# Kernel optimization log

Hardware: AMD Instinct MI355X
Metric: run time of the kernel (lower is better)

The kernel has to match this reference:

```python
import jax, jax.numpy as jnp
import numpy as np

EPS = 1e-5

def conv1d(x, w, b):
    # x: (N,C,L), w: (O,I,3), stride 1, padding 1 -> same length
    y = jax.lax.conv_general_dilated(x, w, window_strides=(1,), padding=((1, 1),),
                                     dimension_numbers=('NCH', 'OIH', 'NCH'))
    return y + b[None, :, None]

def bn(x, g, b):
    # BatchNorm1d, training-mode batch statistics over (N, L) per channel
    m = x.mean(axis=(0, 2), keepdims=True)
    v = x.var(axis=(0, 2), keepdims=True)
    return (x - m) * jax.lax.rsqrt(v + EPS) * g[None, :, None] + b[None, :, None]

def setup_inputs() -> dict:
    V, E, H, L, NL = 50257, 512, 512, 2048, 2
    D = 1 + NL * 2  # 5 channels in the pre-attention conv stack
    key = jax.random.key(0)
    ks = iter(jax.random.split(key, 48))
    def rn(shape, s=0.02):
        return jax.random.normal(next(ks), shape, dtype=jnp.float32) * s
    inp = dict(
        emb=rn((V, E), 1.0),
        conv1_w=rn((32, D, 3)), conv1_b=rn((32,)),
        conv2_w=rn((D, 32, 3)), conv2_b=rn((D,)),
        conv3_w=rn((1, D, 3)), conv3_b=rn((1,)),
        conv4_w=rn((32, 3, 3)), conv4_b=rn((32,)),
        conv5_w=rn((3, 32, 3)), conv5_b=rn((3,)),
        conv6_w=rn((1, 3, 3)), conv6_b=rn((1,)),
        bn1_g=jnp.ones((32,)), bn1_b=jnp.zeros((32,)),
        bn2_g=jnp.ones((D,)), bn2_b=jnp.zeros((D,)),
        bn3_g=jnp.ones((1,)), bn3_b=jnp.zeros((1,)),
        bn4_g=jnp.ones((32,)), bn4_b=jnp.zeros((32,)),
        bn5_g=jnp.ones((3,)), bn5_b=jnp.zeros((3,)),
        bn6_g=jnp.ones((1,)), bn6_b=jnp.zeros((1,)),
        att_w=rn((L, E)), att_b=rn((L,)),
        gru_wih=rn((4, 3 * H, E)), gru_whh=rn((4, 3 * H, H)),
        gru_bih=rn((4, 3 * H)), gru_bhh=rn((4, 3 * H)),
        lo_w=rn((V, H)), lo_b=rn((V,)),
        h_state=rn((4, 1, H), 1.0),
        encoder_outs=rn((L, 2 * H), 1.0),
        x=jax.random.randint(next(ks), (1,), 0, V),
    )
    return inp

def reference(emb, conv1_w, conv1_b, conv2_w, conv2_b, conv3_w, conv3_b,
              conv4_w, conv4_b, conv5_w, conv5_b, conv6_w, conv6_b,
              bn1_g, bn1_b, bn2_g, bn2_b, bn3_g, bn3_b,
              bn4_g, bn4_b, bn5_g, bn5_b, bn6_g, bn6_b,
              att_w, att_b, gru_wih, gru_whh, gru_bih, gru_bhh,
              lo_w, lo_b, h_state, encoder_outs, x):
    H = h_state.shape[-1]
    # dropout(p=0.1) treated as identity (eval mode / deterministic reference)
    embadded = emb[x].reshape(1, 1, H)                                      # (1,1,512)
    pre = jnp.concatenate([h_state.reshape(1, -1, H), embadded], axis=1)    # (1,5,512)
    c = jax.nn.relu(bn(conv1d(pre, conv1_w, conv1_b), bn1_g, bn1_b))        # (1,32,512)
    pre = jax.nn.relu(bn(conv1d(c, conv2_w, conv2_b) + pre, bn2_g, bn2_b))  # residual, (1,5,512)
    pre = jax.nn.relu(bn(conv1d(pre, conv3_w, conv3_b), bn3_g, bn3_b))      # (1,1,512)
    aw = jax.nn.softmax(pre.reshape(1, -1) @ att_w.T + att_b, axis=1)       # (1,L)
    app = (aw @ encoder_outs).reshape(1, -1, H)                             # (1,2,512) (bidir encoder)
    com = jnp.concatenate([app, embadded], axis=1)                          # (1,3,512)
    c = jax.nn.relu(bn(conv1d(com, conv4_w, conv4_b), bn4_g, bn4_b))        # (1,32,512)
    com = jax.nn.relu(bn(conv1d(c, conv5_w, conv5_b) + com, bn5_g, bn5_b))  # residual, (1,3,512)
    com = jax.nn.relu(bn(conv1d(com, conv6_w, conv6_b), bn6_g, bn6_b))      # (1,1,512)
    # 4-layer stacked GRU, single time step, batch 1 (PyTorch gate order r,z,n)
    xt = com.reshape(H)
    h_new = []
    for l in range(h_state.shape[0]):
        gi = gru_wih[l] @ xt + gru_bih[l]
        gh = gru_whh[l] @ h_state[l, 0] + gru_bhh[l]
        ir, iz, inn = jnp.split(gi, 3)
        hr, hz, hn = jnp.split(gh, 3)
        r = jax.nn.sigmoid(ir + hr)
        z = jax.nn.sigmoid(iz + hz)
        n = jnp.tanh(inn + r * hn)
        xt = (1.0 - z) * n + z * h_state[l, 0]
        h_new.append(xt)
    h_state_new = jnp.stack(h_new)[:, None, :]                              # (4,1,512)
    out = jax.nn.log_softmax((xt @ lo_w.T + lo_b)[None, :], axis=1)         # (1,V)
    return out, h_state_new
```

## Files before the change

kernel.cpp:

```cpp
#include <hip/hip_runtime.h>
#include <hip/hip_bf16.h>

typedef __attribute__((ext_vector_type(4))) float f32x4;

constexpr int WSF_PRE1 = 0;
constexpr int WSF_LOGA = 512;
constexpr int WSF_PART = 2560;
constexpr int WSF_SUME = 18944;
constexpr int WSF_XT   = 18960;
constexpr int WSF_LOGV = 21520;
constexpr int WSF_PM   = 71792;
constexpr int WSF_PS   = 72592;
constexpr int WSF_LSE  = 73392;
constexpr int NVOCAB   = 50257;
constexpr int NBLK_V   = 786;

__device__ __forceinline__ float wave_rsum(float v) {
#pragma unroll
    for (int o = 32; o > 0; o >>= 1) v += __shfl_down(v, o);
    return v;
}
__device__ __forceinline__ float sigm(float x) { return 1.0f / (1.0f + __expf(-x)); }

__global__ __launch_bounds__(512) void k_pre(
    const float* __restrict__ emb, const int* __restrict__ xidx,
    const float* __restrict__ hstate,
    const float* __restrict__ w1, const float* __restrict__ b1,
    const float* __restrict__ w2, const float* __restrict__ b2,
    const float* __restrict__ w3, const float* __restrict__ b3,
    const float* __restrict__ g1, const float* __restrict__ bb1,
    const float* __restrict__ g2, const float* __restrict__ bb2,
    const float* __restrict__ g3, const float* __restrict__ bb3,
    float* __restrict__ ws)
{
    constexpr int W1 = 0, B1 = 480, G1 = 512, BB1 = 544;
    constexpr int W2 = 576, B2 = 1056, G2 = 1061, BB2 = 1066;
    constexpr int W3 = 1071, B3 = 1086, G3 = 1087, BB3 = 1088, NW = 1089;
    __shared__ float s_w[NW];
    __shared__ float s_pre[5][512];
    __shared__ float s_y[32][512];
    __shared__ float s_stat[32][2];

    const int tid = threadIdx.x;
    const int lane = tid & 63, wid = tid >> 6;
    const int l = tid;

    if (tid < 480) s_w[W1 + tid] = w1[tid];
    if (tid < 32) { s_w[B1 + tid] = b1[tid]; s_w[G1 + tid] = g1[tid]; s_w[BB1 + tid] = bb1[tid]; }
    if (tid < 480) s_w[W2 + tid] = w2[tid];
    if (tid < 5) { s_w[B2 + tid] = b2[tid]; s_w[G2 + tid] = g2[tid]; s_w[BB2 + tid] = bb2[tid]; }
    if (tid < 15) s_w[W3 + tid] = w3[tid];
    if (tid == 0) { s_w[B3] = b3[0]; s_w[G3] = g3[0]; s_w[BB3] = bb3[0]; }

    const int x = xidx[0];
#pragma unroll
    for (int c = 0; c < 4; ++c) s_pre[c][l] = hstate[c * 512 + l];
    s_pre[4][l] = emb[(size_t)x * 512 + l];
    __syncthreads();

    float px[5][3];
#pragma unroll
    for (int ic = 0; ic < 5; ++ic) {
        px[ic][0] = (l > 0)   ? s_pre[ic][l - 1] : 0.0f;
        px[ic][1] =             s_pre[ic][l];
        px[ic][2] = (l < 511) ? s_pre[ic][l + 1] : 0.0f;
    }
#pragma unroll 4
    for (int oc = 0; oc < 32; ++oc) {
        float a = s_w[B1 + oc];
#pragma unroll
        for (int ic = 0; ic < 5; ++ic)
#pragma unroll
            for (int k = 0; k < 3; ++k)
                a += s_w[W1 + oc * 15 + ic * 3 + k] * px[ic][k];
        s_y[oc][l] = a;
    }
    __syncthreads();

#pragma unroll
    for (int t = 0; t < 4; ++t) {
        const int oc = wid * 4 + t;
        float s = 0.f, s2 = 0.f;
#pragma unroll
        for (int j = 0; j < 8; ++j) {
            float v = s_y[oc][lane + j * 64];
            s += v; s2 += v * v;
        }
        s = wave_rsum(s); s2 = wave_rsum(s2);
        if (lane == 0) {
            float m = s * (1.0f / 512.0f);
            float var = s2 * (1.0f / 512.0f) - m * m;
            s_stat[oc][0] = m; s_stat[oc][1] = rsqrtf(var + 1e-5f);
        }
    }
    __syncthreads();

#pragma unroll 4
    for (int oc = 0; oc < 32; ++oc) {
        float m = s_stat[oc][0], r = s_stat[oc][1];
        s_y[oc][l] = fmaxf((s_y[oc][l] - m) * r * s_w[G1 + oc] + s_w[BB1 + oc], 0.0f);
    }
    __syncthreads();

    float y2[5];
#pragma unroll
    for (int oc = 0; oc < 5; ++oc) y2[oc] = s_w[B2 + oc];
#pragma unroll 2
    for (int ic = 0; ic < 32; ++ic) {
        float c0 = (l > 0)   ? s_y[ic][l - 1] : 0.0f;
        float c1 =             s_y[ic][l];
        float c2 = (l < 511) ? s_y[ic][l + 1] : 0.0f;
#pragma unroll
        for (int oc = 0; oc < 5; ++oc) {
            const int base = W2 + (oc * 32 + ic) * 3;
            y2[oc] += s_w[base] * c0 + s_w[base + 1] * c1 + s_w[base + 2] * c2;
        }
    }
#pragma unroll
    for (int oc = 0; oc < 5; ++oc) y2[oc] += s_pre[oc][l];
    __syncthreads();
#pragma unroll
    for (int oc = 0; oc < 5; ++oc) s_y[oc][l] = y2[oc];
    __syncthreads();

    if (wid < 5) {
        const int oc = wid;
        float s = 0.f, s2 = 0.f;
#pragma unroll
        for (int j = 0; j < 8; ++j) {
            float v = s_y[oc][lane + j * 64];
            s += v; s2 += v * v;
        }
        s = wave_rsum(s); s2 = wave_rsum(s2);
        if (lane == 0) {
            float m = s * (1.0f / 512.0f);
            float var = s2 * (1.0f / 512.0f) - m * m;
            s_stat[oc][0] = m; s_stat[oc][1] = rsqrtf(var + 1e-5f);
        }
    }
    __syncthreads();
#pragma unroll
    for (int oc = 0; oc < 5; ++oc) {
        float m = s_stat[oc][0], r = s_stat[oc][1];
        s_pre[oc][l] = fmaxf((y2[oc] - m) * r * s_w[G2 + oc] + s_w[BB2 + oc], 0.0f);
    }
    __syncthreads();

    float a3 = s_w[B3];
#pragma unroll
    for (int ic = 0; ic < 5; ++ic) {
        float c0 = (l > 0)   ? s_pre[ic][l - 1] : 0.0f;
        float c1 =             s_pre[ic][l];
        float c2 = (l < 511) ? s_pre[ic][l + 1] : 0.0f;
        a3 += s_w[W3 + ic * 3] * c0 + s_w[W3 + ic * 3 + 1] * c1 + s_w[W3 + ic * 3 + 2] * c2;
    }
    s_y[0][l] = a3;
    __syncthreads();
    if (wid == 0) {
        float s = 0.f, s2 = 0.f;
#pragma unroll
        for (int j = 0; j < 8; ++j) {
            float v = s_y[0][lane + j * 64];
            s += v; s2 += v * v;
        }
        s = wave_rsum(s); s2 = wave_rsum(s2);
        if (lane == 0) {
            float m = s * (1.0f / 512.0f);
            float var = s2 * (1.0f / 512.0f) - m * m;
            s_stat[0][0] = m; s_stat[0][1] = rsqrtf(var + 1e-5f);
        }
    }
    __syncthreads();
    ws[WSF_PRE1 + l] = fmaxf((a3 - s_stat[0][0]) * s_stat[0][1] * s_w[G3] + s_w[BB3], 0.0f);
}

__global__ __launch_bounds__(256) void k_attlogit(
    const float* __restrict__ attw, const float* __restrict__ attb,
    float* __restrict__ ws)
{
    const int tid = threadIdx.x, lane = tid & 63, wid = tid >> 6;
    float q0[4], q1[4];
#pragma unroll
    for (int j = 0; j < 4; ++j) {
        q0[j] = ws[WSF_PRE1 + lane * 4 + j];
        q1[j] = ws[WSF_PRE1 + 256 + lane * 4 + j];
    }
    const int row0 = (blockIdx.x * 4 + wid) * 4;
#pragma unroll
    for (int r = 0; r < 4; ++r) {
        const int row = row0 + r;
        f32x4 w0 = *reinterpret_cast<const f32x4*>(attw + (size_t)row * 512 + lane * 4);
        f32x4 w1 = *reinterpret_cast<const f32x4*>(attw + (size_t)row * 512 + 256 + lane * 4);
        float a = 0.f;
#pragma unroll
        for (int j = 0; j < 4; ++j) a += w0[j] * q0[j] + w1[j] * q1[j];
        a = wave_rsum(a);
        if (lane == 0) ws[WSF_LOGA + row] = a + attb[row];
    }
}

__global__ __launch_bounds__(256) void k_attpv(
    const float* __restrict__ enc, float* __restrict__ ws)
{
    __shared__ float s_e[2048];
    __shared__ float s_r[256];
    const int tid = threadIdx.x;
#pragma unroll
    for (int k = 0; k < 8; ++k) s_e[tid + k * 256] = ws[WSF_LOGA + tid + k * 256];
    __syncthreads();
    float m = -INFINITY;
#pragma unroll
    for (int k = 0; k < 8; ++k) m = fmaxf(m, s_e[tid + k * 256]);
    s_r[tid] = m; __syncthreads();
    for (int s = 128; s > 0; s >>= 1) {
        if (tid < s) s_r[tid] = fmaxf(s_r[tid], s_r[tid + s]);
        __syncthreads();
    }
    const float M = s_r[0];
    __syncthreads();
    float t = 0.f;
#pragma unroll
    for (int k = 0; k < 8; ++k) {
        const int i = tid + k * 256;
        float e = __expf(s_e[i] - M);
        s_e[i] = e;
        t += e;
    }
    s_r[tid] = t; __syncthreads();
    for (int s = 128; s > 0; s >>= 1) {
        if (tid < s) s_r[tid] += s_r[tid + s];
        __syncthreads();
    }
    const float S = s_r[0];
    if (blockIdx.x == 0 && tid == 0) ws[WSF_SUME] = S;

    const int jc = blockIdx.x >> 1, half = blockIdx.x & 1;
    const int col = half * 512 + tid * 2;
    const float* ep = enc + (size_t)(jc * 128) * 1024 + col;
    float a0 = 0.f, a1 = 0.f;
#pragma unroll 4
    for (int jj = 0; jj < 128; ++jj) {
        const float w = s_e[jc * 128 + jj];
        float2 e = *reinterpret_cast<const float2*>(ep + (size_t)jj * 1024);
        a0 += w * e.x;
        a1 += w * e.y;
    }
    ws[WSF_PART + jc * 1024 + col]     = a0;
    ws[WSF_PART + jc * 1024 + col + 1] = a1;
}

__global__ __launch_bounds__(512) void k_post(
    const float* __restrict__ emb, const int* __restrict__ xidx,
    const float* __restrict__ w4, const float* __restrict__ b4,
    const float* __restrict__ w5, const float* __restrict__ b5,
    const float* __restrict__ w6, const float* __restrict__ b6,
    const float* __restrict__ g4, const float* __restrict__ bb4,
    const float* __restrict__ g5, const float* __restrict__ bb5,
    const float* __restrict__ g6, const float* __restrict__ bb6,
    float* __restrict__ ws)
{
    constexpr int W4 = 0, B4 = 288, G4 = 320, BB4 = 352;
    constexpr int W5 = 384, B5 = 672, G5 = 675, BB5 = 678;
    constexpr int W6 = 681, B6 = 690, G6 = 691, BB6 = 692, NW = 693;
    __shared__ float s_w[NW];
    __shared__ float s_com[3][512];
    __shared__ float s_y[32][512];
    __shared__ float s_stat[32][2];

    const int tid = threadIdx.x;
    const int lane = tid & 63, wid = tid >> 6;
    const int l = tid;

    if (tid < 288) s_w[W4 + tid] = w4[tid];
    if (tid < 32) { s_w[B4 + tid] = b4[tid]; s_w[G4 + tid] = g4[tid]; s_w[BB4 + tid] = bb4[tid]; }
    if (tid < 288) s_w[W5 + tid] = w5[tid];
    if (tid < 3) { s_w[B5 + tid] = b5[tid]; s_w[G5 + tid] = g5[tid]; s_w[BB5 + tid] = bb5[tid]; }
    if (tid < 9) s_w[W6 + tid] = w6[tid];
    if (tid == 0) { s_w[B6] = b6[0]; s_w[G6] = g6[0]; s_w[BB6] = bb6[0]; }

    const float invS = 1.0f / ws[WSF_SUME];
    float a0 = 0.f, a1 = 0.f;
#pragma unroll
    for (int p = 0; p < 16; ++p) {
        a0 += ws[WSF_PART + p * 1024 + l];
        a1 += ws[WSF_PART + p * 1024 + 512 + l];
    }
    const int x = xidx[0];
    s_com[0][l] = a0 * invS;
    s_com[1][l] = a1 * invS;
    s_com[2][l] = emb[(size_t)x * 512 + l];
    __syncthreads();

    float px[3][3];
#pragma unroll
    for (int ic = 0; ic < 3; ++ic) {
        px[ic][0] = (l > 0)   ? s_com[ic][l - 1] : 0.0f;
        px[ic][1] =             s_com[ic][l];
        px[ic][2] = (l < 511) ? s_com[ic][l + 1] : 0.0f;
    }
#pragma unroll 4
    for (int oc = 0; oc < 32; ++oc) {
        float a = s_w[B4 + oc];
#pragma unroll
        for (int ic = 0; ic < 3; ++ic)
#pragma unroll
            for (int k = 0; k < 3; ++k)
                a += s_w[W4 + oc * 9 + ic * 3 + k] * px[ic][k];
        s_y[oc][l] = a;
    }
    __syncthreads();

#pragma unroll
    for (int t = 0; t < 4; ++t) {
        const int oc = wid * 4 + t;
        float s = 0.f, s2 = 0.f;
#pragma unroll
        for (int j = 0; j < 8; ++j) {
            float v = s_y[oc][lane + j * 64];
            s += v; s2 += v * v;
        }
        s = wave_rsum(s); s2 = wave_rsum(s2);
        if (lane == 0) {
            float m = s * (1.0f / 512.0f);
            float var = s2 * (1.0f / 512.0f) - m * m;
            s_stat[oc][0] = m; s_stat[oc][1] = rsqrtf(var + 1e-5f);
        }
    }
    __syncthreads();
#pragma unroll 4
    for (int oc = 0; oc < 32; ++oc) {
        float m = s_stat[oc][0], r = s_stat[oc][1];
        s_y[oc][l] = fmaxf((s_y[oc][l] - m) * r * s_w[G4 + oc] + s_w[BB4 + oc], 0.0f);
    }
    __syncthreads();

    float y2[3];
#pragma unroll
    for (int oc = 0; oc < 3; ++oc) y2[oc] = s_w[B5 + oc];
#pragma unroll 2
    for (int ic = 0; ic < 32; ++ic) {
        float c0 = (l > 0)   ? s_y[ic][l - 1] : 0.0f;
        float c1 =             s_y[ic][l];
        float c2 = (l < 511) ? s_y[ic][l + 1] : 0.0f;
#pragma unroll
        for (int oc = 0; oc < 3; ++oc) {
            const int base = W5 + (oc * 32 + ic) * 3;
            y2[oc] += s_w[base] * c0 + s_w[base + 1] * c1 + s_w[base + 2] * c2;
        }
    }
#pragma unroll
    for (int oc = 0; oc < 3; ++oc) y2[oc] += s_com[oc][l];
    __syncthreads();
#pragma unroll
    for (int oc = 0; oc < 3; ++oc) s_y[oc][l] = y2[oc];
    __syncthreads();
    if (wid < 3) {
        const int oc = wid;
        float s = 0.f, s2 = 0.f;
#pragma unroll
        for (int j = 0; j < 8; ++j) {
            float v = s_y[oc][lane + j * 64];
            s += v; s2 += v * v;
        }
        s = wave_rsum(s); s2 = wave_rsum(s2);
        if (lane == 0) {
            float m = s * (1.0f / 512.0f);
            float var = s2 * (1.0f / 512.0f) - m * m;
            s_stat[oc][0] = m; s_stat[oc][1] = rsqrtf(var + 1e-5f);
        }
    }
    __syncthreads();
#pragma unroll
    for (int oc = 0; oc < 3; ++oc) {
        float m = s_stat[oc][0], r = s_stat[oc][1];
        s_com[oc][l] = fmaxf((y2[oc] - m) * r * s_w[G5 + oc] + s_w[BB5 + oc], 0.0f);
    }
    __syncthreads();

    float a6 = s_w[B6];
#pragma unroll
    for (int ic = 0; ic < 3; ++ic) {
        float c0 = (l > 0)   ? s_com[ic][l - 1] : 0.0f;
        float c1 =             s_com[ic][l];
        float c2 = (l < 511) ? s_com[ic][l + 1] : 0.0f;
        a6 += s_w[W6 + ic * 3] * c0 + s_w[W6 + ic * 3 + 1] * c1 + s_w[W6 + ic * 3 + 2] * c2;
    }
    s_y[0][l] = a6;
    __syncthreads();
    if (wid == 0) {
        float s = 0.f, s2 = 0.f;
#pragma unroll
        for (int j = 0; j < 8; ++j) {
            float v = s_y[0][lane + j * 64];
            s += v; s2 += v * v;
        }
        s = wave_rsum(s); s2 = wave_rsum(s2);
        if (lane == 0) {
            float m = s * (1.0f / 512.0f);
            float var = s2 * (1.0f / 512.0f) - m * m;
            s_stat[0][0] = m; s_stat[0][1] = rsqrtf(var + 1e-5f);
        }
    }
    __syncthreads();
    ws[WSF_XT + l] = fmaxf((a6 - s_stat[0][0]) * s_stat[0][1] * s_w[G6] + s_w[BB6], 0.0f);
}

__global__ __launch_bounds__(256) void k_gru(
    const float* __restrict__ wih, const float* __restrict__ whh,
    const float* __restrict__ bih, const float* __restrict__ bhh,
    const float* __restrict__ hstate,
    const float* __restrict__ xt_in, float* __restrict__ xt_out,
    float* __restrict__ hout, int layer)
{
    wih += (size_t)layer * 1536 * 512;
    whh += (size_t)layer * 1536 * 512;
    bih += layer * 1536;
    bhh += layer * 1536;
    const float* hp = hstate + layer * 512;

    const int tid = threadIdx.x, lane = tid & 63, wid = tid >> 6;
    float xq0[4], xq1[4], hq0[4], hq1[4];
#pragma unroll
    for (int j = 0; j < 4; ++j) {
        xq0[j] = xt_in[lane * 4 + j];
        xq1[j] = xt_in[256 + lane * 4 + j];
        hq0[j] = hp[lane * 4 + j];
        hq1[j] = hp[256 + lane * 4 + j];
    }
    __shared__ float s_g[8][6];
    const int i0 = blockIdx.x * 8;
#pragma unroll
    for (int t = 0; t < 2; ++t) {
        const int ii = wid * 2 + t;
        const int i = i0 + ii;
        float a[6] = {0.f, 0.f, 0.f, 0.f, 0.f, 0.f};
#pragma unroll
        for (int g = 0; g < 3; ++g) {
            const float* wr = wih + (size_t)(i + g * 512) * 512;
            f32x4 w0 = *reinterpret_cast<const f32x4*>(wr + lane * 4);
            f32x4 w1 = *reinterpret_cast<const f32x4*>(wr + 256 + lane * 4);
#pragma unroll
            for (int j = 0; j < 4; ++j) a[g] += w0[j] * xq0[j] + w1[j] * xq1[j];
        }
#pragma unroll
        for (int g = 0; g < 3; ++g) {
            const float* wr = whh + (size_t)(i + g * 512) * 512;
            f32x4 w0 = *reinterpret_cast<const f32x4*>(wr + lane * 4);
            f32x4 w1 = *reinterpret_cast<const f32x4*>(wr + 256 + lane * 4);
#pragma unroll
            for (int j = 0; j < 4; ++j) a[3 + g] += w0[j] * hq0[j] + w1[j] * hq1[j];
        }
#pragma unroll
        for (int g = 0; g < 6; ++g) a[g] = wave_rsum(a[g]);
        if (lane == 0) {
#pragma unroll
            for (int g = 0; g < 6; ++g) s_g[ii][g] = a[g];
        }
    }
    __syncthreads();
    if (tid < 8) {
        const int i = i0 + tid;
        float ir = s_g[tid][0] + bih[i];
        float iz = s_g[tid][1] + bih[i + 512];
        float in_ = s_g[tid][2] + bih[i + 1024];
        float hr = s_g[tid][3] + bhh[i];
        float hz = s_g[tid][4] + bhh[i + 512];
        float hn = s_g[tid][5] + bhh[i + 1024];
        float r = sigm(ir + hr);
        float z = sigm(iz + hz);
        float n = tanhf(in_ + r * hn);
        float hprev = hp[i];
        float h = (1.0f - z) * n + z * hprev;
        xt_out[i] = h;
        hout[i] = h;
    }
}

__global__ __launch_bounds__(256) void k_vocab(
    const float* __restrict__ low, const float* __restrict__ lob,
    float* __restrict__ ws)
{
    const int tid = threadIdx.x, lane = tid & 63, wid = tid >> 6;
    float q0[4], q1[4];
#pragma unroll
    for (int j = 0; j < 4; ++j) {
        q0[j] = ws[WSF_XT + 4 * 512 + lane * 4 + j];
        q1[j] = ws[WSF_XT + 4 * 512 + 256 + lane * 4 + j];
    }

    const int row0 = blockIdx.x * 64 + wid * 16;
    float m = -INFINITY, s = 0.0f;
#pragma unroll 4
    for (int r = 0; r < 16; ++r) {
        const int row = row0 + r;
        if (row < NVOCAB) {
            f32x4 w0 = *reinterpret_cast<const f32x4*>(low + (size_t)row * 512 + lane * 4);
            f32x4 w1 = *reinterpret_cast<const f32x4*>(low + (size_t)row * 512 + 256 + lane * 4);
            float a = 0.f;
#pragma unroll
            for (int j = 0; j < 4; ++j) a += w0[j] * q0[j] + w1[j] * q1[j];
            a = wave_rsum(a);
            if (lane == 0) {
                float v = a + lob[row];
                ws[WSF_LOGV + row] = v;
                if (v > m) { s = s * __expf(m - v) + 1.0f; m = v; }
                else       { s += __expf(v - m); }
            }
        }
    }
    __shared__ float sm[4], ss[4];
    if (lane == 0) { sm[wid] = m; ss[wid] = s; }
    __syncthreads();
    if (tid == 0) {
        float M = -INFINITY, S = 0.0f;
#pragma unroll
        for (int w = 0; w < 4; ++w) {
            float mb = sm[w], sb = ss[w];
            if (sb > 0.0f) {
                if (mb > M) { S = S * __expf(M - mb) + sb; M = mb; }
                else        { S += sb * __expf(mb - M); }
            }
        }
        ws[WSF_PM + blockIdx.x] = M;
        ws[WSF_PS + blockIdx.x] = S;
    }
}

__global__ __launch_bounds__(256) void k_lse(float* __restrict__ ws, int nb)
{
    __shared__ float sm[256], ss[256];
    const int tid = threadIdx.x;
    float M = -INFINITY, S = 0.0f;
    for (int i = tid; i < nb; i += 256) {
        float mb = ws[WSF_PM + i], sb = ws[WSF_PS + i];
        if (sb > 0.0f) {
            if (mb > M) { S = S * __expf(M - mb) + sb; M = mb; }
            else        { S += sb * __expf(mb - M); }
        }
    }
    sm[tid] = M; ss[tid] = S;
    __syncthreads();
    for (int st = 128; st > 0; st >>= 1) {
        if (tid < st) {
            float mb = sm[tid + st], sb = ss[tid + st];
            if (sb > 0.0f) {
                if (mb > sm[tid]) { ss[tid] = ss[tid] * __expf(sm[tid] - mb) + sb; sm[tid] = mb; }
                else              { ss[tid] += sb * __expf(mb - sm[tid]); }
            }
        }
        __syncthreads();
    }
    if (tid == 0) ws[WSF_LSE] = sm[0] + logf(ss[0]);
}

__global__ __launch_bounds__(256) void k_out(
    const float* __restrict__ ws, float* __restrict__ out)
{
    const int i = blockIdx.x * 256 + threadIdx.x;
    if (i < NVOCAB) out[i] = ws[WSF_LOGV + i] - ws[WSF_LSE];
}

extern "C" void kernel_launch(void* const* d_in, const int* in_sizes, int n_in,
                              void* d_out, int out_size, void* d_ws, size_t ws_size,
                              hipStream_t stream)
{
    (void)in_sizes; (void)n_in; (void)out_size; (void)ws_size;
    const float* emb     = (const float*)d_in[0];
    const float* conv1_w = (const float*)d_in[1];  const float* conv1_b = (const float*)d_in[2];
    const float* conv2_w = (const float*)d_in[3];  const float* conv2_b = (const float*)d_in[4];
    const float* conv3_w = (const float*)d_in[5];  const float* conv3_b = (const float*)d_in[6];
    const float* conv4_w = (const float*)d_in[7];  const float* conv4_b = (const float*)d_in[8];
    const float* conv5_w = (const float*)d_in[9];  const float* conv5_b = (const float*)d_in[10];
    const float* conv6_w = (const float*)d_in[11]; const float* conv6_b = (const float*)d_in[12];
    const float* bn1_g = (const float*)d_in[13];   const float* bn1_b = (const float*)d_in[14];
    const float* bn2_g = (const float*)d_in[15];   const float* bn2_b = (const float*)d_in[16];
    const float* bn3_g = (const float*)d_in[17];   const float* bn3_b = (const float*)d_in[18];
    const float* bn4_g = (const float*)d_in[19];   const float* bn4_b = (const float*)d_in[20];
    const float* bn5_g = (const float*)d_in[21];   const float* bn5_b = (const float*)d_in[22];
    const float* bn6_g = (const float*)d_in[23];   const float* bn6_b = (const float*)d_in[24];
    const float* att_w = (const float*)d_in[25];   const float* att_b = (const float*)d_in[26];
    const float* gru_wih = (const float*)d_in[27]; const float* gru_whh = (const float*)d_in[28];
    const float* gru_bih = (const float*)d_in[29]; const float* gru_bhh = (const float*)d_in[30];
    const float* lo_w = (const float*)d_in[31];    const float* lo_b = (const float*)d_in[32];
    const float* h_state = (const float*)d_in[33];
    const float* enc = (const float*)d_in[34];
    const int* x = (const int*)d_in[35];

    float* ws = (float*)d_ws;
    float* out = (float*)d_out;

    k_pre<<<1, 512, 0, stream>>>(emb, x, h_state,
        conv1_w, conv1_b, conv2_w, conv2_b, conv3_w, conv3_b,
        bn1_g, bn1_b, bn2_g, bn2_b, bn3_g, bn3_b, ws);
    k_attlogit<<<128, 256, 0, stream>>>(att_w, att_b, ws);
    k_attpv<<<32, 256, 0, stream>>>(enc, ws);
    k_post<<<1, 512, 0, stream>>>(emb, x,
        conv4_w, conv4_b, conv5_w, conv5_b, conv6_w, conv6_b,
        bn4_g, bn4_b, bn5_g, bn5_b, bn6_g, bn6_b, ws);
    for (int l = 0; l < 4; ++l) {
        k_gru<<<64, 256, 0, stream>>>(gru_wih, gru_whh, gru_bih, gru_bhh, h_state,
            ws + WSF_XT + l * 512, ws + WSF_XT + (l + 1) * 512,
            out + NVOCAB + l * 512, l);
    }
    k_vocab<<<NBLK_V, 256, 0, stream>>>(lo_w, lo_b, ws);
    k_lse<<<1, 256, 0, stream>>>(ws, NBLK_V);
    k_out<<<197, 256, 0, stream>>>(ws, out);
}
```

Before: 100.4 us.

## Fuse attention logits with PV and merge LSE into output kernel

Merges the attention-logit and attention-PV kernels into one kernel in which each block computes exp of its 64 logits, writes a partial denominator and accumulates its partial context vector. The global max subtraction is dropped. The vocab LSE reduction is folded into the output kernel, with every block recomputing it redundantly. This removes two launches and a global serialization step, at the cost of fewer blocks streaming att_w and possible exp overflow for large logits.

```diff
diff --git a/kernel.cpp b/kernel.cpp
--- a/kernel.cpp
+++ b/kernel.cpp
@@ -3,17 +3,15 @@
 
 typedef __attribute__((ext_vector_type(4))) float f32x4;
 
-constexpr int WSF_PRE1 = 0;
-constexpr int WSF_LOGA = 512;
-constexpr int WSF_PART = 2560;
-constexpr int WSF_SUME = 18944;
-constexpr int WSF_XT   = 18960;
-constexpr int WSF_LOGV = 21520;
-constexpr int WSF_PM   = 71792;
-constexpr int WSF_PS   = 72592;
-constexpr int WSF_LSE  = 73392;
-constexpr int NVOCAB   = 50257;
-constexpr int NBLK_V   = 786;
+constexpr int WSF_Q     = 0;
+constexpr int WSF_ADEN  = 512;
+constexpr int WSF_APART = 1024;
+constexpr int WSF_XT    = 33792;
+constexpr int WSF_LOGV  = 36352;
+constexpr int WSF_PM    = 86624;
+constexpr int WSF_PS    = 87424;
+constexpr int NVOCAB    = 50257;
+constexpr int NBLK_V    = 786;
 
 __device__ __forceinline__ float wave_rsum(float v) {
 #pragma unroll
@@ -40,10 +38,7 @@
     __shared__ float s_pre[5][512];
     __shared__ float s_y[32][512];
     __shared__ float s_stat[32][2];
-
-    const int tid = threadIdx.x;
-    const int lane = tid & 63, wid = tid >> 6;
-    const int l = tid;
+    const int tid = threadIdx.x, lane = tid & 63, wid = tid >> 6, l = tid;
 
     if (tid < 480) s_w[W1 + tid] = w1[tid];
     if (tid < 32) { s_w[B1 + tid] = b1[tid]; s_w[G1 + tid] = g1[tid]; s_w[BB1 + tid] = bb1[tid]; }
@@ -61,9 +56,9 @@
     float px[5][3];
 #pragma unroll
     for (int ic = 0; ic < 5; ++ic) {
-        px[ic][0] = (l > 0)   ? s_pre[ic][l - 1] : 0.0f;
+        px[ic][0] = (l > 0)   ? s_pre[ic][l-1] : 0.f;
         px[ic][1] =             s_pre[ic][l];
-        px[ic][2] = (l < 511) ? s_pre[ic][l + 1] : 0.0f;
+        px[ic][2] = (l < 511) ? s_pre[ic][l+1] : 0.f;
     }
 #pragma unroll 4
     for (int oc = 0; oc < 32; ++oc) {
@@ -72,34 +67,23 @@
         for (int ic = 0; ic < 5; ++ic)
 #pragma unroll
             for (int k = 0; k < 3; ++k)
-                a += s_w[W1 + oc * 15 + ic * 3 + k] * px[ic][k];
+                a += s_w[W1 + oc*15 + ic*3 + k] * px[ic][k];
         s_y[oc][l] = a;
     }
     __syncthreads();
-
 #pragma unroll
     for (int t = 0; t < 4; ++t) {
         const int oc = wid * 4 + t;
         float s = 0.f, s2 = 0.f;
 #pragma unroll
-        for (int j = 0; j < 8; ++j) {
-            float v = s_y[oc][lane + j * 64];
-            s += v; s2 += v * v;
-        }
+        for (int j = 0; j < 8; ++j) { float v = s_y[oc][lane + j*64]; s += v; s2 += v*v; }
         s = wave_rsum(s); s2 = wave_rsum(s2);
-        if (lane == 0) {
-            float m = s * (1.0f / 512.0f);
-            float var = s2 * (1.0f / 512.0f) - m * m;
-            s_stat[oc][0] = m; s_stat[oc][1] = rsqrtf(var + 1e-5f);
-        }
-    }
-    __syncthreads();
-
+        if (lane == 0) { float m = s/512.f, var = s2/512.f - m*m; s_stat[oc][0] = m; s_stat[oc][1] = rsqrtf(var + 1e-5f); }
+    }
+    __syncthreads();
 #pragma unroll 4
-    for (int oc = 0; oc < 32; ++oc) {
-        float m = s_stat[oc][0], r = s_stat[oc][1];
-        s_y[oc][l] = fmaxf((s_y[oc][l] - m) * r * s_w[G1 + oc] + s_w[BB1 + oc], 0.0f);
-    }
+    for (int oc = 0; oc < 32; ++oc)
+        s_y[oc][l] = fmaxf((s_y[oc][l] - s_stat[oc][0]) * s_stat[oc][1] * s_w[G1+oc] + s_w[BB1+oc], 0.f);
     __syncthreads();
 
     float y2[5];
@@ -107,13 +91,13 @@
     for (int oc = 0; oc < 5; ++oc) y2[oc] = s_w[B2 + oc];
 #pragma unroll 2
     for (int ic = 0; ic < 32; ++ic) {
-        float c0 = (l > 0)   ? s_y[ic][l - 1] : 0.0f;
+        float c0 = (l > 0)   ? s_y[ic][l-1] : 0.f;
         float c1 =             s_y[ic][l];
-        float c2 = (l < 511) ? s_y[ic][l + 1] : 0.0f;
+        float c2 = (l < 511) ? s_y[ic][l+1] : 0.f;
 #pragma unroll
         for (int oc = 0; oc < 5; ++oc) {
-            const int base = W2 + (oc * 32 + ic) * 3;
-            y2[oc] += s_w[base] * c0 + s_w[base + 1] * c1 + s_w[base + 2] * c2;
+            const int base = W2 + (oc*32 + ic)*3;
+            y2[oc] += s_w[base]*c0 + s_w[base+1]*c1 + s_w[base+2]*c2;
         }
     }
 #pragma unroll
@@ -122,131 +106,85 @@
 #pragma unroll
     for (int oc = 0; oc < 5; ++oc) s_y[oc][l] = y2[oc];
     __syncthreads();
-
     if (wid < 5) {
         const int oc = wid;
         float s = 0.f, s2 = 0.f;
 #pragma unroll
-        for (int j = 0; j < 8; ++j) {
-            float v = s_y[oc][lane + j * 64];
-            s += v; s2 += v * v;
-        }
+        for (int j = 0; j < 8; ++j) { float v = s_y[oc][lane + j*64]; s += v; s2 += v*v; }
         s = wave_rsum(s); s2 = wave_rsum(s2);
-        if (lane == 0) {
-            float m = s * (1.0f / 512.0f);
-            float var = s2 * (1.0f / 512.0f) - m * m;
-            s_stat[oc][0] = m; s_stat[oc][1] = rsqrtf(var + 1e-5f);
-        }
-    }
-    __syncthreads();
-#pragma unroll
-    for (int oc = 0; oc < 5; ++oc) {
-        float m = s_stat[oc][0], r = s_stat[oc][1];
-        s_pre[oc][l] = fmaxf((y2[oc] - m) * r * s_w[G2 + oc] + s_w[BB2 + oc], 0.0f);
-    }
+        if (lane == 0) { float m = s/512.f, var = s2/512.f - m*m; s_stat[oc][0] = m; s_stat[oc][1] = rsqrtf(var + 1e-5f); }
+    }
+    __syncthreads();
+#pragma unroll
+    for (int oc = 0; oc < 5; ++oc)
+        s_pre[oc][l] = fmaxf((y2[oc] - s_stat[oc][0]) * s_stat[oc][1] * s_w[G2+oc] + s_w[BB2+oc], 0.f);
     __syncthreads();
 
     float a3 = s_w[B3];
 #pragma unroll
     for (int ic = 0; ic < 5; ++ic) {
-        float c0 = (l > 0)   ? s_pre[ic][l - 1] : 0.0f;
+        float c0 = (l > 0)   ? s_pre[ic][l-1] : 0.f;
         float c1 =             s_pre[ic][l];
-        float c2 = (l < 511) ? s_pre[ic][l + 1] : 0.0f;
-        a3 += s_w[W3 + ic * 3] * c0 + s_w[W3 + ic * 3 + 1] * c1 + s_w[W3 + ic * 3 + 2] * c2;
+        float c2 = (l < 511) ? s_pre[ic][l+1] : 0.f;
+        a3 += s_w[W3+ic*3]*c0 + s_w[W3+ic*3+1]*c1 + s_w[W3+ic*3+2]*c2;
     }
     s_y[0][l] = a3;
     __syncthreads();
     if (wid == 0) {
         float s = 0.f, s2 = 0.f;
 #pragma unroll
-        for (int j = 0; j < 8; ++j) {
-            float v = s_y[0][lane + j * 64];
-            s += v; s2 += v * v;
-        }
+        for (int j = 0; j < 8; ++j) { float v = s_y[0][lane + j*64]; s += v; s2 += v*v; }
         s = wave_rsum(s); s2 = wave_rsum(s2);
+        if (lane == 0) { float m = s/512.f, var = s2/512.f - m*m; s_stat[0][0] = m; s_stat[0][1] = rsqrtf(var + 1e-5f); }
+    }
+    __syncthreads();
+    ws[WSF_Q + l] = fmaxf((a3 - s_stat[0][0]) * s_stat[0][1] * s_w[G3] + s_w[BB3], 0.f);
+}
+
+__global__ __launch_bounds__(256) void k_att(
+    const float* __restrict__ attw, const float* __restrict__ attb,
+    const float* __restrict__ enc, float* __restrict__ ws)
+{
+    __shared__ float s_e[64];
+    __shared__ float s_d[4];
+    const int tid = threadIdx.x, lane = tid & 63, wid = tid >> 6;
+    const int jc = blockIdx.x;
+
+    float q0[4], q1[4];
+#pragma unroll
+    for (int j = 0; j < 4; ++j) {
+        q0[j] = ws[WSF_Q + lane*4 + j];
+        q1[j] = ws[WSF_Q + 256 + lane*4 + j];
+    }
+    float dpart = 0.f;
+#pragma unroll 4
+    for (int r = 0; r < 16; ++r) {
+        const int row = jc * 64 + wid * 16 + r;
+        f32x4 w0 = *(const f32x4*)(attw + (size_t)row*512 + lane*4);
+        f32x4 w1 = *(const f32x4*)(attw + (size_t)row*512 + 256 + lane*4);
+        float a = 0.f;
+#pragma unroll
+        for (int j = 0; j < 4; ++j) a += w0[j]*q0[j] + w1[j]*q1[j];
+        a = wave_rsum(a);
         if (lane == 0) {
-            float m = s * (1.0f / 512.0f);
-            float var = s2 * (1.0f / 512.0f) - m * m;
-            s_stat[0][0] = m; s_stat[0][1] = rsqrtf(var + 1e-5f);
-        }
-    }
-    __syncthreads();
-    ws[WSF_PRE1 + l] = fmaxf((a3 - s_stat[0][0]) * s_stat[0][1] * s_w[G3] + s_w[BB3], 0.0f);
-}
-
-__global__ __launch_bounds__(256) void k_attlogit(
-    const float* __restrict__ attw, const float* __restrict__ attb,
-    float* __restrict__ ws)
-{
-    const int tid = threadIdx.x, lane = tid & 63, wid = tid >> 6;
-    float q0[4], q1[4];
-#pragma unroll
-    for (int j = 0; j < 4; ++j) {
-        q0[j] = ws[WSF_PRE1 + lane * 4 + j];
-        q1[j] = ws[WSF_PRE1 + 256 + lane * 4 + j];
-    }
-    const int row0 = (blockIdx.x * 4 + wid) * 4;
-#pragma unroll
-    for (int r = 0; r < 4; ++r) {
-        const int row = row0 + r;
-        f32x4 w0 = *reinterpret_cast<const f32x4*>(attw + (size_t)row * 512 + lane * 4);
-        f32x4 w1 = *reinterpret_cast<const f32x4*>(attw + (size_t)row * 512 + 256 + lane * 4);
-        float a = 0.f;
-#pragma unroll
-        for (int j = 0; j < 4; ++j) a += w0[j] * q0[j] + w1[j] * q1[j];
-        a = wave_rsum(a);
-        if (lane == 0) ws[WSF_LOGA + row] = a + attb[row];
-    }
-}
-
-__global__ __launch_bounds__(256) void k_attpv(
-    const float* __restrict__ enc, float* __restrict__ ws)
-{
-    __shared__ float s_e[2048];
-    __shared__ float s_r[256];
-    const int tid = threadIdx.x;
-#pragma unroll
-    for (int k = 0; k < 8; ++k) s_e[tid + k * 256] = ws[WSF_LOGA + tid + k * 256];
-    __syncthreads();
-    float m = -INFINITY;
-#pragma unroll
-    for (int k = 0; k < 8; ++k) m = fmaxf(m, s_e[tid + k * 256]);
-    s_r[tid] = m; __syncthreads();
-    for (int s = 128; s > 0; s >>= 1) {
-        if (tid < s) s_r[tid] = fmaxf(s_r[tid], s_r[tid + s]);
-        __syncthreads();
-    }
-    const float M = s_r[0];
-    __syncthreads();
-    float t = 0.f;
-#pragma unroll
-    for (int k = 0; k < 8; ++k) {
-        const int i = tid + k * 256;
-        float e = __expf(s_e[i] - M);
-        s_e[i] = e;
-        t += e;
-    }
-    s_r[tid] = t; __syncthreads();
-    for (int s = 128; s > 0; s >>= 1) {
-        if (tid < s) s_r[tid] += s_r[tid + s];
-        __syncthreads();
-    }
-    const float S = s_r[0];
-    if (blockIdx.x == 0 && tid == 0) ws[WSF_SUME] = S;
-
-    const int jc = blockIdx.x >> 1, half = blockIdx.x & 1;
-    const int col = half * 512 + tid * 2;
-    const float* ep = enc + (size_t)(jc * 128) * 1024 + col;
-    float a0 = 0.f, a1 = 0.f;
-#pragma unroll 4
-    for (int jj = 0; jj < 128; ++jj) {
-        const float w = s_e[jc * 128 + jj];
-        float2 e = *reinterpret_cast<const float2*>(ep + (size_t)jj * 1024);
-        a0 += w * e.x;
-        a1 += w * e.y;
-    }
-    ws[WSF_PART + jc * 1024 + col]     = a0;
-    ws[WSF_PART + jc * 1024 + col + 1] = a1;
+            float e = __expf(a + attb[row]);
+            s_e[wid*16 + r] = e;
+            dpart += e;
+        }
+    }
+    if (lane == 0) s_d[wid] = dpart;
+    __syncthreads();
+    if (tid == 0) ws[WSF_ADEN + jc] = s_d[0] + s_d[1] + s_d[2] + s_d[3];
+
+    const int col = tid * 4;
+    const float* ep = enc + (size_t)(jc * 64) * 1024 + col;
+    f32x4 acc = {0.f, 0.f, 0.f, 0.f};
+#pragma unroll 8
+    for (int jj = 0; jj < 64; ++jj) {
+        f32x4 v = *(const f32x4*)(ep + (size_t)jj * 1024);
+        acc += s_e[jj] * v;
+    }
+    *(f32x4*)(ws + WSF_APART + jc * 1024 + col) = acc;
 }
 
 __global__ __launch_bounds__(512) void k_post(
@@ -266,10 +204,7 @@
     __shared__ float s_com[3][512];
     __shared__ float s_y[32][512];
     __shared__ float s_stat[32][2];
-
-    const int tid = threadIdx.x;
-    const int lane = tid & 63, wid = tid >> 6;
-    const int l = tid;
+    const int tid = threadIdx.x, lane = tid & 63, wid = tid >> 6, l = tid;
 
     if (tid < 288) s_w[W4 + tid] = w4[tid];
     if (tid < 32) { s_w[B4 + tid] = b4[tid]; s_w[G4 + tid] = g4[tid]; s_w[BB4 + tid] = bb4[tid]; }
@@ -278,25 +213,28 @@
     if (tid < 9) s_w[W6 + tid] = w6[tid];
     if (tid == 0) { s_w[B6] = b6[0]; s_w[G6] = g6[0]; s_w[BB6] = bb6[0]; }
 
-    const float invS = 1.0f / ws[WSF_SUME];
+    float den = 0.f;
+#pragma unroll 8
+    for (int i = 0; i < 32; ++i) den += ws[WSF_ADEN + i];
+    const float invS = 1.0f / den;
     float a0 = 0.f, a1 = 0.f;
-#pragma unroll
-    for (int p = 0; p < 16; ++p) {
-        a0 += ws[WSF_PART + p * 1024 + l];
-        a1 += ws[WSF_PART + p * 1024 + 512 + l];
+#pragma unroll 8
+    for (int p = 0; p < 32; ++p) {
+        a0 += ws[WSF_APART + p*1024 + l];
+        a1 += ws[WSF_APART + p*1024 + 512 + l];
     }
     const int x = xidx[0];
     s_com[0][l] = a0 * invS;
     s_com[1][l] = a1 * invS;
-    s_com[2][l] = emb[(size_t)x * 512 + l];
+    s_com[2][l] = emb[(size_t)x*512 + l];
     __syncthreads();
 
     float px[3][3];
 #pragma unroll
     for (int ic = 0; ic < 3; ++ic) {
-        px[ic][0] = (l > 0)   ? s_com[ic][l - 1] : 0.0f;
+        px[ic][0] = (l > 0)   ? s_com[ic][l-1] : 0.f;
         px[ic][1] =             s_com[ic][l];
-        px[ic][2] = (l < 511) ? s_com[ic][l + 1] : 0.0f;
+        px[ic][2] = (l < 511) ? s_com[ic][l+1] : 0.f;
     }
 #pragma unroll 4
     for (int oc = 0; oc < 32; ++oc) {
@@ -305,33 +243,23 @@
         for (int ic = 0; ic < 3; ++ic)
 #pragma unroll
             for (int k = 0; k < 3; ++k)
-                a += s_w[W4 + oc * 9 + ic * 3 + k] * px[ic][k];
+                a += s_w[W4 + oc*9 + ic*3 + k] * px[ic][k];
         s_y[oc][l] = a;
     }
     __syncthreads();
-
 #pragma unroll
     for (int t = 0; t < 4; ++t) {
         const int oc = wid * 4 + t;
         float s = 0.f, s2 = 0.f;
 #pragma unroll
-        for (int j = 0; j < 8; ++j) {
-            float v = s_y[oc][lane + j * 64];
-            s += v; s2 += v * v;
-        }
+        for (int j = 0; j < 8; ++j) { float v = s_y[oc][lane + j*64]; s += v; s2 += v*v; }
         s = wave_rsum(s); s2 = wave_rsum(s2);
-        if (lane == 0) {
-            float m = s * (1.0f / 512.0f);
-            float var = s2 * (1.0f / 512.0f) - m * m;
-            s_stat[oc][0] = m; s_stat[oc][1] = rsqrtf(var + 1e-5f);
-        }
+        if (lane == 0) { float m = s/512.f, var = s2/512.f - m*m; s_stat[oc][0] = m; s_stat[oc][1] = rsqrtf(var + 1e-5f); }
     }
     __syncthreads();
 #pragma unroll 4
-    for (int oc = 0; oc < 32; ++oc) {
-        float m = s_stat[oc][0], r = s_stat[oc][1];
-        s_y[oc][l] = fmaxf((s_y[oc][l] - m) * r * s_w[G4 + oc] + s_w[BB4 + oc], 0.0f);
-    }
+    for (int oc = 0; oc < 32; ++oc)
+        s_y[oc][l] = fmaxf((s_y[oc][l] - s_stat[oc][0]) * s_stat[oc][1] * s_w[G4+oc] + s_w[BB4+oc], 0.f);
     __syncthreads();
 
     float y2[3];
@@ -339,13 +267,13 @@
     for (int oc = 0; oc < 3; ++oc) y2[oc] = s_w[B5 + oc];
 #pragma unroll 2
     for (int ic = 0; ic < 32; ++ic) {
-        float c0 = (l > 0)   ? s_y[ic][l - 1] : 0.0f;
+        float c0 = (l > 0)   ? s_y[ic][l-1] : 0.f;
         float c1 =             s_y[ic][l];
-        float c2 = (l < 511) ? s_y[ic][l + 1] : 0.0f;
+        float c2 = (l < 511) ? s_y[ic][l+1] : 0.f;
 #pragma unroll
         for (int oc = 0; oc < 3; ++oc) {
-            const int base = W5 + (oc * 32 + ic) * 3;
-            y2[oc] += s_w[base] * c0 + s_w[base + 1] * c1 + s_w[base + 2] * c2;
+            const int base = W5 + (oc*32 + ic)*3;
+            y2[oc] += s_w[base]*c0 + s_w[base+1]*c1 + s_w[base+2]*c2;
         }
     }
 #pragma unroll
@@ -358,51 +286,35 @@
         const int oc = wid;
         float s = 0.f, s2 = 0.f;
 #pragma unroll
-        for (int j = 0; j < 8; ++j) {
-            float v = s_y[oc][lane + j * 64];
-            s += v; s2 += v * v;
-        }
+        for (int j = 0; j < 8; ++j) { float v = s_y[oc][lane + j*64]; s += v; s2 += v*v; }
         s = wave_rsum(s); s2 = wave_rsum(s2);
-        if (lane == 0) {
-            float m = s * (1.0f / 512.0f);
-            float var = s2 * (1.0f / 512.0f) - m * m;
-            s_stat[oc][0] = m; s_stat[oc][1] = rsqrtf(var + 1e-5f);
-        }
-    }
-    __syncthreads();
-#pragma unroll
-    for (int oc = 0; oc < 3; ++oc) {
-        float m = s_stat[oc][0], r = s_stat[oc][1];
-        s_com[oc][l] = fmaxf((y2[oc] - m) * r * s_w[G5 + oc] + s_w[BB5 + oc], 0.0f);
-    }
+        if (lane == 0) { float m = s/512.f, var = s2/512.f - m*m; s_stat[oc][0] = m; s_stat[oc][1] = rsqrtf(var + 1e-5f); }
+    }
+    __syncthreads();
+#pragma unroll
+    for (int oc = 0; oc < 3; ++oc)
+        s_com[oc][l] = fmaxf((y2[oc] - s_stat[oc][0]) * s_stat[oc][1] * s_w[G5+oc] + s_w[BB5+oc], 0.f);
     __syncthreads();
 
     float a6 = s_w[B6];
 #pragma unroll
     for (int ic = 0; ic < 3; ++ic) {
-        float c0 = (l > 0)   ? s_com[ic][l - 1] : 0.0f;
+        float c0 = (l > 0)   ? s_com[ic][l-1] : 0.f;
         float c1 =             s_com[ic][l];
-        float c2 = (l < 511) ? s_com[ic][l + 1] : 0.0f;
-        a6 += s_w[W6 + ic * 3] * c0 + s_w[W6 + ic * 3 + 1] * c1 + s_w[W6 + ic * 3 + 2] * c2;
+        float c2 = (l < 511) ? s_com[ic][l+1] : 0.f;
+        a6 += s_w[W6+ic*3]*c0 + s_w[W6+ic*3+1]*c1 + s_w[W6+ic*3+2]*c2;
     }
     s_y[0][l] = a6;
     __syncthreads();
     if (wid == 0) {
         float s = 0.f, s2 = 0.f;
 #pragma unroll
-        for (int j = 0; j < 8; ++j) {
-            float v = s_y[0][lane + j * 64];
-            s += v; s2 += v * v;
-        }
+        for (int j = 0; j < 8; ++j) { float v = s_y[0][lane + j*64]; s += v; s2 += v*v; }
         s = wave_rsum(s); s2 = wave_rsum(s2);
-        if (lane == 0) {
-            float m = s * (1.0f / 512.0f);
-            float var = s2 * (1.0f / 512.0f) - m * m;
-            s_stat[0][0] = m; s_stat[0][1] = rsqrtf(var + 1e-5f);
-        }
-    }
-    __syncthreads();
-    ws[WSF_XT + l] = fmaxf((a6 - s_stat[0][0]) * s_stat[0][1] * s_w[G6] + s_w[BB6], 0.0f);
+        if (lane == 0) { float m = s/512.f, var = s2/512.f - m*m; s_stat[0][0] = m; s_stat[0][1] = rsqrtf(var + 1e-5f); }
+    }
+    __syncthreads();
+    ws[WSF_XT + l] = fmaxf((a6 - s_stat[0][0]) * s_stat[0][1] * s_w[G6] + s_w[BB6], 0.f);
 }
 
 __global__ __launch_bounds__(256) void k_gru(
@@ -422,10 +334,10 @@
     float xq0[4], xq1[4], hq0[4], hq1[4];
 #pragma unroll
     for (int j = 0; j < 4; ++j) {
-        xq0[j] = xt_in[lane * 4 + j];
-        xq1[j] = xt_in[256 + lane * 4 + j];
-        hq0[j] = hp[lane * 4 + j];
-        hq1[j] = hp[256 + lane * 4 + j];
+        xq0[j] = xt_in[lane*4 + j];
+        xq1[j] = xt_in[256 + lane*4 + j];
+        hq0[j] = hp[lane*4 + j];
+        hq1[j] = hp[256 + lane*4 + j];
     }
     __shared__ float s_g[8][6];
     const int i0 = blockIdx.x * 8;
@@ -436,19 +348,19 @@
         float a[6] = {0.f, 0.f, 0.f, 0.f, 0.f, 0.f};
 #pragma unroll
         for (int g = 0; g < 3; ++g) {
-            const float* wr = wih + (size_t)(i + g * 512) * 512;
-            f32x4 w0 = *reinterpret_cast<const f32x4*>(wr + lane * 4);
-            f32x4 w1 = *reinterpret_cast<const f32x4*>(wr + 256 + lane * 4);
-#pragma unroll
-            for (int j = 0; j < 4; ++j) a[g] += w0[j] * xq0[j] + w1[j] * xq1[j];
+            const float* wr = wih + (size_t)(i + g*512) * 512;
+            f32x4 w0 = *(const f32x4*)(wr + lane*4);
+            f32x4 w1 = *(const f32x4*)(wr + 256 + lane*4);
+#pragma unroll
+            for (int j = 0; j < 4; ++j) a[g] += w0[j]*xq0[j] + w1[j]*xq1[j];
         }
 #pragma unroll
         for (int g = 0; g < 3; ++g) {
-            const float* wr = whh + (size_t)(i + g * 512) * 512;
-            f32x4 w0 = *reinterpret_cast<const f32x4*>(wr + lane * 4);
-            f32x4 w1 = *reinterpret_cast<const f32x4*>(wr + 256 + lane * 4);
-#pragma unroll
-            for (int j = 0; j < 4; ++j) a[3 + g] += w0[j] * hq0[j] + w1[j] * hq1[j];
+            const float* wr = whh + (size_t)(i + g*512) * 512;
+            f32x4 w0 = *(const f32x4*)(wr + lane*4);
+            f32x4 w1 = *(const f32x4*)(wr + 256 + lane*4);
+#pragma unroll
+            for (int j = 0; j < 4; ++j) a[3+g] += w0[j]*hq0[j] + w1[j]*hq1[j];
         }
 #pragma unroll
         for (int g = 0; g < 6; ++g) a[g] = wave_rsum(a[g]);
@@ -469,8 +381,7 @@
         float r = sigm(ir + hr);
         float z = sigm(iz + hz);
         float n = tanhf(in_ + r * hn);
-        float hprev = hp[i];
-        float h = (1.0f - z) * n + z * hprev;
+        float h = (1.f - z) * n + z * hp[i];
         xt_out[i] = h;
         hout[i] = h;
     }
@@ -484,21 +395,20 @@
     float q0[4], q1[4];
 #pragma unroll
     for (int j = 0; j < 4; ++j) {
-        q0[j] = ws[WSF_XT + 4 * 512 + lane * 4 + j];
-        q1[j] = ws[WSF_XT + 4 * 512 + 256 + lane * 4 + j];
-    }
-
+        q0[j] = ws[WSF_XT + 4*512 + lane*4 + j];
+        q1[j] = ws[WSF_XT + 4*512 + 256 + lane*4 + j];
+    }
     const int row0 = blockIdx.x * 64 + wid * 16;
     float m = -INFINITY, s = 0.0f;
 #pragma unroll 4
     for (int r = 0; r < 16; ++r) {
         const int row = row0 + r;
         if (row < NVOCAB) {
-            f32x4 w0 = *reinterpret_cast<const f32x4*>(low + (size_t)row * 512 + lane * 4);
-            f32x4 w1 = *reinterpret_cast<const f32x4*>(low + (size_t)row * 512 + 256 + lane * 4);
+            f32x4 w0 = *(const f32x4*)(low + (size_t)row*512 + lane*4);
+            f32x4 w1 = *(const f32x4*)(low + (size_t)row*512 + 256 + lane*4);
             float a = 0.f;
 #pragma unroll
-            for (int j = 0; j < 4; ++j) a += w0[j] * q0[j] + w1[j] * q1[j];
+            for (int j = 0; j < 4; ++j) a += w0[j]*q0[j] + w1[j]*q1[j];
             a = wave_rsum(a);
             if (lane == 0) {
                 float v = a + lob[row];
@@ -508,14 +418,14 @@
             }
         }
     }
-    __shared__ float sm[4], ss[4];
-    if (lane == 0) { sm[wid] = m; ss[wid] = s; }
+    __shared__ float smx[4], ssx[4];
+    if (lane == 0) { smx[wid] = m; ssx[wid] = s; }
     __syncthreads();
     if (tid == 0) {
         float M = -INFINITY, S = 0.0f;
 #pragma unroll
         for (int w = 0; w < 4; ++w) {
-            float mb = sm[w], sb = ss[w];
+            float mb = smx[w], sb = ssx[w];
             if (sb > 0.0f) {
                 if (mb > M) { S = S * __expf(M - mb) + sb; M = mb; }
                 else        { S += sb * __expf(mb - M); }
@@ -526,38 +436,32 @@
     }
 }
 
-__global__ __launch_bounds__(256) void k_lse(float* __restrict__ ws, int nb)
-{
-    __shared__ float sm[256], ss[256];
+__global__ __launch_bounds__(256) void k_outlse(
+    const float* __restrict__ ws, float* __restrict__ out)
+{
+    __shared__ float smx[256], ssx[256];
     const int tid = threadIdx.x;
     float M = -INFINITY, S = 0.0f;
-    for (int i = tid; i < nb; i += 256) {
+    for (int i = tid; i < NBLK_V; i += 256) {
         float mb = ws[WSF_PM + i], sb = ws[WSF_PS + i];
-        if (sb > 0.0f) {
-            if (mb > M) { S = S * __expf(M - mb) + sb; M = mb; }
-            else        { S += sb * __expf(mb - M); }
-        }
-    }
-    sm[tid] = M; ss[tid] = S;
+        if (mb > M) { S = S * __expf(M - mb) + sb; M = mb; }
+        else        { S += sb * __expf(mb - M); }
+    }
+    smx[tid] = M; ssx[tid] = S;
     __syncthreads();
     for (int st = 128; st > 0; st >>= 1) {
         if (tid < st) {
-            float mb = sm[tid + st], sb = ss[tid + st];
+            float mb = smx[tid + st], sb = ssx[tid + st];
             if (sb > 0.0f) {
-                if (mb > sm[tid]) { ss[tid] = ss[tid] * __expf(sm[tid] - mb) + sb; sm[tid] = mb; }
-                else              { ss[tid] += sb * __expf(mb - sm[tid]); }
+                if (mb > smx[tid]) { ssx[tid] = ssx[tid] * __expf(smx[tid] - mb) + sb; smx[tid] = mb; }
+                else               { ssx[tid] += sb * __expf(mb - smx[tid]); }
             }
         }
         __syncthreads();
     }
-    if (tid == 0) ws[WSF_LSE] = sm[0] + logf(ss[0]);
-}
-
-__global__ __launch_bounds__(256) void k_out(
-    const float* __restrict__ ws, float* __restrict__ out)
-{
-    const int i = blockIdx.x * 256 + threadIdx.x;
-    if (i < NVOCAB) out[i] = ws[WSF_LOGV + i] - ws[WSF_LSE];
+    const float lse = smx[0] + logf(ssx[0]);
+    const int i = blockIdx.x * 256 + tid;
+    if (i < NVOCAB) out[i] = ws[WSF_LOGV + i] - lse;
 }
 
 extern "C" void kernel_launch(void* const* d_in, const int* in_sizes, int n_in,
@@ -592,8 +496,7 @@
     k_pre<<<1, 512, 0, stream>>>(emb, x, h_state,
         conv1_w, conv1_b, conv2_w, conv2_b, conv3_w, conv3_b,
         bn1_g, bn1_b, bn2_g, bn2_b, bn3_g, bn3_b, ws);
-    k_attlogit<<<128, 256, 0, stream>>>(att_w, att_b, ws);
-    k_attpv<<<32, 256, 0, stream>>>(enc, ws);
+    k_att<<<32, 256, 0, stream>>>(att_w, att_b, enc, ws);
     k_post<<<1, 512, 0, stream>>>(emb, x,
         conv4_w, conv4_b, conv5_w, conv5_b, conv6_w, conv6_b,
         bn4_g, bn4_b, bn5_g, bn5_b, bn6_g, bn6_b, ws);
@@ -603,6 +506,5 @@
             out + NVOCAB + l * 512, l);
     }
     k_vocab<<<NBLK_V, 256, 0, stream>>>(lo_w, lo_b, ws);
-    k_lse<<<1, 256, 0, stream>>>(ws, NBLK_V);
-    k_out<<<197, 256, 0, stream>>>(ws, out);
-}
+    k_outlse<<<197, 256, 0, stream>>>(ws, out);
+}
```

Result: faster. 96.56 us (-3.8%).
